# Performance work log

Hardware: AMD Instinct MI355X
Metric: run time of the kernel (lower is better)

The kernel has to match this reference:

```python
import jax, jax.numpy as jnp
import numpy as np

# Model dims (rexgen/WLN canonical hyperparameters)
B, N, MAXNB, NBONDS = 16, 100, 10, 120
AF, BF, H, BIN = 82, 6, 300, 11
DEPTH, K = 3, 80


def setup_inputs() -> dict:
    key = jax.random.key(0)
    ks = jax.random.split(key, 24)
    f32 = jnp.float32
    inp = {}
    inp["fatoms"] = jax.random.normal(ks[0], (B, N, AF), f32)
    inp["fbonds"] = jax.random.normal(ks[1], (B, NBONDS, BF), f32)
    inp["atom_nb"] = jax.random.randint(ks[2], (B, N, MAXNB), 0, N)
    inp["bond_nb"] = jax.random.randint(ks[3], (B, N, MAXNB), 0, NBONDS)
    inp["num_nbs"] = jnp.full((B, N), MAXNB, jnp.int32)
    inp["n_atoms"] = jnp.full((B,), N, jnp.int32)
    inp["binary_feats"] = jax.random.normal(ks[4], (B, N, N, BIN), f32)
    inp["mask_neis"] = (jax.random.uniform(ks[5], (B, N, MAXNB, 1)) > 0.2).astype(f32)
    inp["mask_atoms"] = jnp.ones((B, N, 1), f32)
    # sparse_idx enumerates all (sample, atom_i, atom_j) pairs in row-major order
    sb = jnp.repeat(jnp.arange(B), N * N)
    si = jnp.tile(jnp.repeat(jnp.arange(N), N), B)
    sj = jnp.tile(jnp.arange(N), B * N)
    inp["sparse_idx"] = jnp.stack([sb, si, sj], axis=1).astype(jnp.int32)

    def w(k, shape):
        return jax.random.normal(k, shape, f32) * 0.1

    # WLNet params
    inp["W_atom"] = w(ks[6], (AF, H))
    inp["W_nei_atom"] = w(ks[7], (H, H))
    inp["W_nei_bond"] = w(ks[8], (BF, H))
    inp["W_self"] = w(ks[9], (H, H))
    inp["W_U2"] = w(ks[10], (H + BF, H)); inp["b_U2"] = jnp.zeros((H,), f32)
    inp["W_U1"] = w(ks[11], (2 * H, H)); inp["b_U1"] = jnp.zeros((H,), f32)
    # Attention params
    inp["W_att_local"] = w(ks[12], (H, H))
    inp["W_att_bin"] = w(ks[13], (BIN, H)); inp["b_att"] = jnp.zeros((H,), f32)
    inp["W_att_score"] = w(ks[14], (H, 1)); inp["b_att_score"] = jnp.zeros((1,), f32)
    # ReactivityScoring params
    inp["W_pl"] = w(ks[15], (H, H))
    inp["W_pg"] = w(ks[16], (H, H))
    inp["W_pb"] = w(ks[17], (BIN, H)); inp["b_p"] = jnp.zeros((H,), f32)
    inp["W_out"] = w(ks[18], (H, 1)); inp["b_out"] = jnp.zeros((1,), f32)
    return inp


def _pair_scores(fatoms, fbonds, binary_feats, mask_neis, mask_atoms,
                 W_atom, W_nei_atom, W_nei_bond, W_self, W_U2, b_U2, W_U1, b_U1,
                 W_att_local, W_att_bin, b_att, W_att_score, b_att_score,
                 W_pl, W_pg, W_pb, b_p, W_out, b_out,
                 atom_nb, bond_nb, sparse_idx):
    bidx = jnp.arange(B)[:, None, None]
    # --- WLNet graph convolution ---
    h = jax.nn.relu(fatoms @ W_atom)                       # [B,N,H]
    local = h
    for _ in range(DEPTH):
        fnei_atom = h[bidx, atom_nb]                       # [B,N,MAXNB,H]
        fnei_bond = fbonds[bidx, bond_nb]                  # [B,N,MAXNB,BF]
        h_nei = (fnei_atom @ W_nei_atom) * (fnei_bond @ W_nei_bond)
        f_nei = (h_nei * mask_neis).sum(axis=2)            # [B,N,H]
        f_self = h @ W_self
        local = f_nei * f_self * mask_atoms                # kernel output
        nei_label = jax.nn.relu(jnp.concatenate([fnei_atom, fnei_bond], -1) @ W_U2 + b_U2)
        nei_label = (nei_label * mask_neis).sum(axis=2)
        h = jax.nn.relu(jnp.concatenate([h, nei_label], -1) @ W_U1 + b_U1)
    # --- Global attention over atom pairs ---
    pair = local[:, :, None, :] + local[:, None, :, :]     # [B,N,N,H]
    att_h = jax.nn.relu(pair @ W_att_local + binary_feats @ W_att_bin + b_att)
    att_s = jax.nn.sigmoid(att_h @ W_att_score + b_att_score)  # [B,N,N,1]
    ctx = jnp.einsum('bij,bjh->bih', att_s[..., 0], local)     # [B,N,H]
    # --- Gather sparse pairs and score reactivity ---
    sb, si, sj = sparse_idx[:, 0], sparse_idx[:, 1], sparse_idx[:, 2]
    local_pair = local[sb, si] + local[sb, sj]             # [P,H]
    global_pair = ctx[sb, si] + ctx[sb, sj]                # [P,H]
    bin_pair = binary_feats[sb, si, sj]                    # [P,BIN]
    hid = jax.nn.relu(local_pair @ W_pl + global_pair @ W_pg + bin_pair @ W_pb + b_p)
    return hid @ W_out + b_out                             # [P,1]


def reference(fatoms, fbonds, atom_nb, bond_nb, num_nbs, n_atoms, binary_feats,
              mask_neis, mask_atoms, sparse_idx,
              W_atom, W_nei_atom, W_nei_bond, W_self, W_U2, b_U2, W_U1, b_U1,
              W_att_local, W_att_bin, b_att, W_att_score, b_att_score,
              W_pl, W_pg, W_pb, b_p, W_out, b_out):
    pair_scores = _pair_scores(fatoms, fbonds, binary_feats, mask_neis, mask_atoms,
                               W_atom, W_nei_atom, W_nei_bond, W_self, W_U2, b_U2, W_U1, b_U1,
                               W_att_local, W_att_bin, b_att, W_att_score, b_att_score,
                               W_pl, W_pg, W_pb, b_p, W_out, b_out,
                               atom_nb, bond_nb, sparse_idx)
    # Segmented top-k: sparse_idx rows are grouped & ordered by sample with
    # exactly N*N pairs each, so per-sample flatten == reshape to [B, N*N].
    _, topks = jax.lax.top_k(pair_scores.reshape(B, N * N), K)  # indices, matching torch.topk[1]
    return pair_scores, topks
```

## Files before the change

### kernel.cpp

```cpp
#include <hip/hip_runtime.h>
#include <hip/hip_bf16.h>
#include <math.h>

#define BB 16
#define NN 100
#define MAXNB 10
#define NBONDS 120
#define AF 82
#define BF 6
#define HH 300
#define BIN 11
#define DEPTH 3
#define KTOP 80

typedef __attribute__((ext_vector_type(8))) short short8;
typedef __attribute__((ext_vector_type(4))) float floatx4;

__device__ __forceinline__ unsigned short f2bf(float f) {
    unsigned int u = __float_as_uint(f);
    unsigned int r = (u + 0x7FFFu + ((u >> 16) & 1u)) >> 16;
    return (unsigned short)r;
}
__device__ __forceinline__ float bf2f(unsigned short h) {
    return __uint_as_float(((unsigned int)h) << 16);
}

#define O_WATOM 0
#define O_WNB   29184
#define O_U2B   38912
#define O_WNA   48640
#define O_P1    145920
#define O_P2    243200
#define O_U1CAT 340480
#define O_WATT  535040
#define O_WPL   632320
#define O_WPG   729600

__global__ __launch_bounds__(256) void k_prep(
    const float* __restrict__ s0, const float* __restrict__ s1,
    const float* __restrict__ s2, const float* __restrict__ s3,
    const float* __restrict__ s4, const float* __restrict__ s5,
    const float* __restrict__ s6, const float* __restrict__ s7,
    const float* __restrict__ s8, const float* __restrict__ s9,
    const float* __restrict__ s10,
    unsigned short* __restrict__ WTh, unsigned short* __restrict__ WTl,
    const float* __restrict__ fatoms, const float* __restrict__ fbonds,
    unsigned short* __restrict__ fatomsbf, unsigned short* __restrict__ fbondsbf,
    const float* __restrict__ bin, unsigned short* __restrict__ BINBF,
    const float* __restrict__ Wbin0, const float* __restrict__ Wbin1,
    unsigned short* __restrict__ WBF0, unsigned short* __restrict__ WBF1)
{
    const int z = blockIdx.z;
    if (z == 11) {
        int idx = blockIdx.x * 256 + threadIdx.x;
        if (idx < 1600 * 96) {
            int r = idx / 96, c = idx - r * 96;
            float f = (c < AF) ? fatoms[r * AF + c] : 0.f;
            unsigned short hb = f2bf(f);
            fatomsbf[r * 192 + c]      = hb;
            fatomsbf[r * 192 + 96 + c] = f2bf(f - bf2f(hb));
        } else {
            int i2 = idx - 1600 * 96;
            if (i2 < 1920 * 32) {
                int r = i2 / 32, c = i2 - r * 32;
                float f = (c < BF) ? fbonds[r * BF + c] : 0.f;
                unsigned short hb = f2bf(f);
                fbondsbf[r * 64 + c]      = hb;
                fbondsbf[r * 64 + 32 + c] = f2bf(f - bf2f(hb));
            }
        }
        return;
    }
    if (z == 12) {
        const int bx = blockIdx.x;
        if (bx < 625) {
            int p = bx * 256 + threadIdx.x;
            if (p < BB * NN * NN) {
                const float* src = bin + (size_t)p * BIN;
                unsigned short tmp[16];
#pragma unroll
                for (int k = 0; k < BIN; k++) tmp[k] = f2bf(src[k]);
#pragma unroll
                for (int k = BIN; k < 16; k++) tmp[k] = 0;
                *(uint4*)(BINBF + (size_t)p * 16) = *(uint4*)tmp;
                *(uint4*)(BINBF + (size_t)p * 16 + 8) = *(uint4*)(tmp + 8);
            }
        } else if (bx < 663) {
            int zb = bx - 625;
            const float* src = (zb >= 19) ? Wbin1 : Wbin0;
            unsigned short* dst = (zb >= 19) ? WBF1 : WBF0;
            int idx = (zb % 19) * 256 + threadIdx.x;
            int jj = idx & 7;
            int koct = (idx >> 3) & 1;
            int n = (idx >> 4) & 15;
            int ch = idx >> 8;
            int k = koct * 8 + jj;
            int h = ch * 16 + n;
            float f = (k < BIN && h < 300) ? src[k * 300 + h] : 0.f;
            dst[idx] = f2bf(f);
        }
        return;
    }
    const float* src; int K, kc, off, u1base = -1;
    switch (z) {
        case 0:  src = s0;  K = AF;  kc = 3;  off = O_WATOM; break;
        case 1:  src = s1;  K = BF;  kc = 1;  off = O_WNB;   break;
        case 2:  src = s2;  K = BF;  kc = 1;  off = O_U2B;   break;
        case 3:  src = s3;  K = HH;  kc = 10; off = O_WNA;   break;
        case 4:  src = s4;  K = HH;  kc = 10; off = O_P1;    break;
        case 5:  src = s5;  K = HH;  kc = 10; off = O_P2;    break;
        case 6:  src = s6;  K = HH;  kc = 10; off = O_U1CAT; u1base = 0;  break;
        case 7:  src = s7;  K = HH;  kc = 10; off = O_U1CAT; u1base = 10; break;
        case 8:  src = s8;  K = HH;  kc = 10; off = O_WATT;  break;
        case 9:  src = s9;  K = HH;  kc = 10; off = O_WPL;   break;
        default: src = s10; K = HH;  kc = 10; off = O_WPG;   break;
    }
    const int lim = 9728 * kc;
    int i = blockIdx.x * 256 + threadIdx.x;
    if (i < lim) {
        int jj = i & 7;
        int lane = (i >> 3) & 63;
        int rem = i >> 9;
        int kci = rem % kc;
        int ct = rem / kc;
        int k = kci * 32 + (lane >> 4) * 8 + jj;
        int col = ct * 16 + (lane & 15);
        float f = (k < K && col < 300) ? src[k * 300 + col] : 0.f;
        unsigned short hb = f2bf(f);
        int dsti = (u1base >= 0)
                 ? off + ct * 10240 + (kci + u1base) * 512 + lane * 8 + jj
                 : off + i;
        WTh[dsti] = hb;
        WTl[dsti] = f2bf(f - bf2f(hb));
    }
}

__device__ __forceinline__ void gemm_epilogue(
    floatx4 acc, int ct, int m, int rq, int row0,
    float* __restrict__ C, int ldc, const float* __restrict__ bias,
    int act, unsigned short* __restrict__ Cbf, int gcolBase)
{
    const int col = ct * 16 + m;
    if (col >= 300) return;
    const float bv = bias ? bias[col] : 0.f;
    const int gcol = gcolBase + col;
#pragma unroll
    for (int r = 0; r < 4; r++) {
        const int grow = row0 + rq * 4 + r;
        float v = acc[r] + bv;
        if (act) v = fmaxf(v, 0.f);
        if (C) C[(size_t)grow * ldc + gcol] = v;
        if (Cbf) {
            unsigned short hb = f2bf(v);
            Cbf[(size_t)grow * 640 + col]       = hb;
            Cbf[(size_t)grow * 640 + 320 + col] = f2bf(v - bf2f(hb));
        }
    }
}

template<int KC>
__device__ __forceinline__ void gemm_core32(
    const unsigned short* __restrict__ A, int lda, int M,
    const unsigned short* __restrict__ wthB, const unsigned short* __restrict__ wtlB,
    float* __restrict__ C, int ldc,
    const float* __restrict__ bias,
    int act, unsigned short* __restrict__ Cbf,
    int row0, int gcolBase)
{
    constexpr int sR = KC * 64 + 8;
    __shared__ unsigned short sa[32 * sR];
    if (row0 >= M) return;
    const int tid = threadIdx.x;
    const int lane = tid & 63;
    const int wid = tid >> 6;

    {
        const uint4* Ag = (const uint4*)A;
        uint4* sa4 = (uint4*)sa;
        constexpr int q4 = KC * 8;
        const int lda4 = lda >> 3;
        constexpr int sR4 = q4 + 1;
        for (int i = tid; i < 32 * q4; i += 256) {
            int r = i / q4, q = i - r * q4;
            sa4[r * sR4 + q] = Ag[(size_t)(row0 + r) * lda4 + q];
        }
    }
    __syncthreads();

    const int ct = blockIdx.y * 4 + wid;
    if (ct >= 19) return;

    const int m = lane & 15;
    const int rq = lane >> 4;
    const int koct8 = rq * 8;
    const unsigned short* wth = wthB + (size_t)ct * KC * 512;
    const unsigned short* wtl = wtlB + (size_t)ct * KC * 512;

    floatx4 acc0 = {0.f, 0.f, 0.f, 0.f};
    floatx4 acc1 = {0.f, 0.f, 0.f, 0.f};
    for (int kci = 0; kci < KC; kci++) {
        short8 ah0 = *(const short8*)(sa + m * sR + kci * 32 + koct8);
        short8 al0 = *(const short8*)(sa + m * sR + KC * 32 + kci * 32 + koct8);
        short8 ah1 = *(const short8*)(sa + (16 + m) * sR + kci * 32 + koct8);
        short8 al1 = *(const short8*)(sa + (16 + m) * sR + KC * 32 + kci * 32 + koct8);
        short8 wh = *(const short8*)(wth + (kci * 64 + lane) * 8);
        short8 wl = *(const short8*)(wtl + (kci * 64 + lane) * 8);
        acc0 = __builtin_amdgcn_mfma_f32_16x16x32_bf16(ah0, wl, acc0, 0, 0, 0);
        acc1 = __builtin_amdgcn_mfma_f32_16x16x32_bf16(ah1, wl, acc1, 0, 0, 0);
        acc0 = __builtin_amdgcn_mfma_f32_16x16x32_bf16(al0, wh, acc0, 0, 0, 0);
        acc1 = __builtin_amdgcn_mfma_f32_16x16x32_bf16(al1, wh, acc1, 0, 0, 0);
        acc0 = __builtin_amdgcn_mfma_f32_16x16x32_bf16(ah0, wh, acc0, 0, 0, 0);
        acc1 = __builtin_amdgcn_mfma_f32_16x16x32_bf16(ah1, wh, acc1, 0, 0, 0);
    }

    gemm_epilogue(acc0, ct, m, rq, row0,      C, ldc, bias, act, Cbf, gcolBase);
    gemm_epilogue(acc1, ct, m, rq, row0 + 16, C, ldc, bias, act, Cbf, gcolBase);
}

__global__ __launch_bounds__(256) void k_gemm_mfma(
    const unsigned short* __restrict__ A, int lda, int M,
    const unsigned short* __restrict__ WTh, const unsigned short* __restrict__ WTl,
    int wtStride,
    float* __restrict__ C, int ldc,
    const float* __restrict__ bias,
    int act, unsigned short* __restrict__ Cbf)
{
    const int widx = blockIdx.z;
    gemm_core32<10>(A, lda, M,
              WTh + (size_t)widx * wtStride, WTl + (size_t)widx * wtStride,
              C, ldc, bias, act, Cbf,
              blockIdx.x * 32, widx * 300);
}

__global__ __launch_bounds__(256) void k_gemm_u1(
    const unsigned short* __restrict__ Ah,
    const unsigned short* __restrict__ An,
    const unsigned short* __restrict__ WTh, const unsigned short* __restrict__ WTl,
    const float* __restrict__ bias,
    unsigned short* __restrict__ Cbf)
{
    __shared__ unsigned short sa[16 * 1288];
    const int row0 = blockIdx.x * 16;
    if (row0 >= 1600) return;
    const int tid = threadIdx.x;
    const int lane = tid & 63;
    const int wid = tid >> 6;

    {
        const uint4* Ag = (const uint4*)Ah;
        const uint4* Ng = (const uint4*)An;
        uint4* sa4 = (uint4*)sa;
        for (int i = tid; i < 16 * 160; i += 256) {
            int r = i / 160, q = i - r * 160;
            const size_t rb = (size_t)(row0 + r) * 80;
            uint4 v;
            if (q < 40)       v = Ag[rb + q];
            else if (q < 80)  v = Ng[rb + (q - 40)];
            else if (q < 120) v = Ag[rb + (q - 40)];
            else              v = Ng[rb + (q - 80)];
            sa4[r * 161 + q] = v;
        }
    }
    __syncthreads();

    const int ct = blockIdx.y * 4 + wid;
    if (ct >= 19) return;

    const int m = lane & 15;
    const int rq = lane >> 4;
    const int koct8 = rq * 8;
    const unsigned short* wth = WTh + (size_t)ct * 10240;
    const unsigned short* wtl = WTl + (size_t)ct * 10240;

    floatx4 acc = {0.f, 0.f, 0.f, 0.f};
    for (int kci = 0; kci < 20; kci++) {
        short8 ah = *(const short8*)(sa + m * 1288 + kci * 32 + koct8);
        short8 al = *(const short8*)(sa + m * 1288 + 640 + kci * 32 + koct8);
        short8 wh = *(const short8*)(wth + (kci * 64 + lane) * 8);
        short8 wl = *(const short8*)(wtl + (kci * 64 + lane) * 8);
        acc = __builtin_amdgcn_mfma_f32_16x16x32_bf16(ah, wl, acc, 0, 0, 0);
        acc = __builtin_amdgcn_mfma_f32_16x16x32_bf16(al, wh, acc, 0, 0, 0);
        acc = __builtin_amdgcn_mfma_f32_16x16x32_bf16(ah, wh, acc, 0, 0, 0);
    }

    const int col = ct * 16 + m;
    if (col < 300) {
        const float bv = bias[col];
#pragma unroll
        for (int r = 0; r < 4; r++) {
            const int grow = row0 + rq * 4 + r;
            float v = fmaxf(acc[r] + bv, 0.f);
            unsigned short hb = f2bf(v);
            Cbf[(size_t)grow * 640 + col]       = hb;
            Cbf[(size_t)grow * 640 + 320 + col] = f2bf(v - bf2f(hb));
        }
    }
}

__global__ __launch_bounds__(256) void k_gemm_first(
    const unsigned short* __restrict__ fatomsbf,
    const unsigned short* __restrict__ fbondsbf,
    const unsigned short* __restrict__ WTh, const unsigned short* __restrict__ WTl,
    unsigned short* __restrict__ hbf, float* __restrict__ FBout)
{
    const int z = blockIdx.z;
    if (z == 0) {
        gemm_core32<3>(fatomsbf, 192, 1600,
                  WTh + O_WATOM, WTl + O_WATOM,
                  nullptr, 0, nullptr, 1, hbf,
                  blockIdx.x * 32, 0);
    } else {
        const int w = z - 1;
        gemm_core32<1>(fbondsbf, 64, 1920,
                  WTh + O_WNB + w * 9728, WTl + O_WNB + w * 9728,
                  FBout, 600, nullptr, 0, nullptr,
                  blockIdx.x * 32, w * 300);
    }
}

__global__ __launch_bounds__(320, 4) void k_neighbor(
    const float* __restrict__ HW, const float* __restrict__ FB,
    const int* __restrict__ atom_nb, const int* __restrict__ bond_nb,
    const float* __restrict__ mask_neis, const float* __restrict__ mask_atoms,
    const float* __restrict__ b_U2,
    unsigned short* __restrict__ localbf, unsigned short* __restrict__ nlbf,
    int computeU1)
{
    __shared__ int   sAn[2][MAXNB];
    __shared__ int   sBd[2][MAXNB];
    __shared__ float sM[2][MAXNB];
    __shared__ float pF[2][300];
    __shared__ float pN[2][300];
    const int tx = threadIdx.x;
    const int ty = threadIdx.y;
    const int tz = threadIdx.z;
    const int bx = blockIdx.x;
    const int bn0 = ((bx & 15) * 50 + (bx >> 4)) * 2;
    const int flat = (tz * 2 + ty) * 80 + tx;

    if (flat < 20)       sAn[flat / 10][flat % 10] = atom_nb[(bn0 + flat / 10) * MAXNB + flat % 10];
    else if (flat < 40)  { int f = flat - 20; sBd[f / 10][f % 10] = bond_nb[(bn0 + f / 10) * MAXNB + f % 10]; }
    else if (flat < 60)  { int f = flat - 40; sM[f / 10][f % 10]  = mask_neis[(bn0 + f / 10) * MAXNB + f % 10]; }
    __syncthreads();

    const int bn = bn0 + ty;
    const int b = bn / NN;
    const int h4 = tx;
    const float4* HW4 = (const float4*)HW;
    const float4* FB4 = (const float4*)FB;

    float4 fnei = make_float4(0.f, 0.f, 0.f, 0.f);
    float4 nls  = fnei;
    if (tx < 75) {
        if (computeU1) {
            const float4 bu = ((const float4*)b_U2)[h4];
#pragma unroll
            for (int kk = 0; kk < 5; kk++) {
                const int k = tz * 5 + kk;
                const int an = sAn[ty][k];
                const int bd = sBd[ty][k];
                const float m = sM[ty][k];
                const float4* hr = HW4 + (size_t)(b * NN + an) * 225;
                const float4* fr = FB4 + (size_t)(b * NBONDS + bd) * 150;
                float4 ha = hr[h4];
                float4 hu = hr[150 + h4];
                float4 fa = fr[h4];
                float4 fu = fr[75 + h4];
                fnei.x = fmaf(m, ha.x * fa.x, fnei.x);
                fnei.y = fmaf(m, ha.y * fa.y, fnei.y);
                fnei.z = fmaf(m, ha.z * fa.z, fnei.z);
                fnei.w = fmaf(m, ha.w * fa.w, fnei.w);
                float ux = hu.x + fu.x + bu.x;
                float uy = hu.y + fu.y + bu.y;
                float uz = hu.z + fu.z + bu.z;
                float uw = hu.w + fu.w + bu.w;
                nls.x = fmaf(m, fmaxf(ux, 0.f), nls.x);
                nls.y = fmaf(m, fmaxf(uy, 0.f), nls.y);
                nls.z = fmaf(m, fmaxf(uz, 0.f), nls.z);
                nls.w = fmaf(m, fmaxf(uw, 0.f), nls.w);
            }
        } else {
#pragma unroll
            for (int kk = 0; kk < 5; kk++) {
                const int k = tz * 5 + kk;
                const int an = sAn[ty][k];
                const int bd = sBd[ty][k];
                const float m = sM[ty][k];
                float4 ha = HW4[(size_t)(b * NN + an) * 225 + h4];
                float4 fa = FB4[(size_t)(b * NBONDS + bd) * 150 + h4];
                fnei.x = fmaf(m, ha.x * fa.x, fnei.x);
                fnei.y = fmaf(m, ha.y * fa.y, fnei.y);
                fnei.z = fmaf(m, ha.z * fa.z, fnei.z);
                fnei.w = fmaf(m, ha.w * fa.w, fnei.w);
            }
        }
        if (tz == 1) {
            ((float4*)pF[ty])[h4] = fnei;
            if (computeU1) ((float4*)pN[ty])[h4] = nls;
        }
    }
    __syncthreads();

    if (tx < 75 && tz == 0) {
        const float4 pf = ((const float4*)pF[ty])[h4];
        fnei.x += pf.x; fnei.y += pf.y; fnei.z += pf.z; fnei.w += pf.w;

        const float ma = mask_atoms[bn];
        const float4 sf = HW4[(size_t)bn * 225 + 75 + h4];
        float lv[4];
        lv[0] = fnei.x * sf.x * ma; lv[1] = fnei.y * sf.y * ma;
        lv[2] = fnei.z * sf.z * ma; lv[3] = fnei.w * sf.w * ma;

        ushort4 lh, ll;
        unsigned short* lhp = (unsigned short*)&lh;
        unsigned short* llp = (unsigned short*)&ll;
#pragma unroll
        for (int c = 0; c < 4; c++) {
            unsigned short hb = f2bf(lv[c]);
            lhp[c] = hb; llp[c] = f2bf(lv[c] - bf2f(hb));
        }
        *(ushort4*)(localbf + (size_t)bn * 640 + h4 * 4)       = lh;
        *(ushort4*)(localbf + (size_t)bn * 640 + 320 + h4 * 4) = ll;

        if (computeU1) {
            const float4 pn = ((const float4*)pN[ty])[h4];
            float nv[4] = {nls.x + pn.x, nls.y + pn.y, nls.z + pn.z, nls.w + pn.w};
            ushort4 nh, nl2;
            unsigned short* nhp = (unsigned short*)&nh;
            unsigned short* nlp = (unsigned short*)&nl2;
#pragma unroll
            for (int c = 0; c < 4; c++) {
                unsigned short nb = f2bf(nv[c]);
                nhp[c] = nb; nlp[c] = f2bf(nv[c] - bf2f(nb));
            }
            *(ushort4*)(nlbf + (size_t)bn * 640 + h4 * 4)       = nh;
            *(ushort4*)(nlbf + (size_t)bn * 640 + 320 + h4 * 4) = nl2;
        }
    }
}

__global__ __launch_bounds__(256) void k_pair(
    const float* __restrict__ R, int ldr,
    const unsigned short* __restrict__ BINBF,
    const unsigned short* __restrict__ WBF,
    const float* __restrict__ bvec,
    const float* __restrict__ Wscore, const float* __restrict__ bscore,
    float* __restrict__ outp, int mode)
{
    __shared__ float sLi[16 * 308];
    __shared__ float sLj[16 * 308];

    const int b  = blockIdx.x;
    const int i0 = blockIdx.y * 16;
    const int j0 = blockIdx.z * 16;
    const int tid = threadIdx.x;
    const int lane = tid & 63;
    const int wid = tid >> 6;

    for (int idx = tid; idx < 16 * 308; idx += 256) {
        int r = idx / 308;
        int c = idx - r * 308;
        float vi = 0.f, vj = 0.f;
        if (c < 300) {
            if (i0 + r < NN) vi = R[(size_t)(b * NN + i0 + r) * ldr + c] + bvec[c];
            if (j0 + r < NN) vj = R[(size_t)(b * NN + j0 + r) * ldr + c];
        }
        sLi[idx] = vi;
        sLj[idx] = vj;
    }

    const int m = lane & 15;
    const int koct = lane >> 4;
    short8 afrag[4];
#pragma unroll
    for (int g = 0; g < 4; g++) {
        int ii = i0 + wid * 4 + g; if (ii > NN - 1) ii = NN - 1;
        int jj2 = j0 + m;          if (jj2 > NN - 1) jj2 = NN - 1;
        const size_t pidx = (size_t)((b * NN + ii) * NN + jj2);
        afrag[g] = *(const short8*)(BINBF + pidx * 16 + (koct & 1) * 8);
        if (koct >= 2) afrag[g] = short8{0,0,0,0,0,0,0,0};
    }
    __syncthreads();

    const int n = lane & 15;
    const int rquad = lane >> 4;
    const floatx4 zero = {0.f, 0.f, 0.f, 0.f};
    float su[4][4];
#pragma unroll
    for (int g = 0; g < 4; g++)
#pragma unroll
        for (int r = 0; r < 4; r++) su[g][r] = 0.f;

    for (int ch = 0; ch < 19; ch++) {
        const int h0 = ch * 16;
        short8 bfrag = {0,0,0,0,0,0,0,0};
        if (lane < 32)
            bfrag = *(const short8*)(WBF + ch * 256 + (n * 2 + koct) * 8);
        float wsv = 0.f;
        if (h0 + n < 300) wsv = Wscore[h0 + n];
#pragma unroll
        for (int g = 0; g < 4; g++) {
            floatx4 P = __builtin_amdgcn_mfma_f32_16x16x32_bf16(
                afrag[g], bfrag, zero, 0, 0, 0);
            const float liv = sLi[(wid * 4 + g) * 308 + h0 + n];
#pragma unroll
            for (int r = 0; r < 4; r++) {
                const float ljv = sLj[(rquad * 4 + r) * 308 + h0 + n];
                float u = P[r] + liv + ljv;
                su[g][r] = fmaf(fmaxf(u, 0.f), wsv, su[g][r]);
            }
        }
    }

    const float bs = bscore[0];
#pragma unroll
    for (int g = 0; g < 4; g++) {
#pragma unroll
        for (int r = 0; r < 4; r++) {
            float v = su[g][r];
            v += __shfl_xor(v, 1);
            v += __shfl_xor(v, 2);
            v += __shfl_xor(v, 4);
            v += __shfl_xor(v, 8);
            if (n == 0) {
                const int i = i0 + wid * 4 + g;
                const int j = j0 + rquad * 4 + r;
                if (i < NN && j < NN) {
                    float s = v + bs;
                    outp[(size_t)(b * NN + i) * NN + j] =
                        (mode == 0) ? (1.f / (1.f + expf(-s))) : s;
                }
            }
        }
    }
}

__global__ __launch_bounds__(320, 2) void k_ctx(
    const float* __restrict__ att, const float* __restrict__ LL,
    float* __restrict__ LPG)
{
    const int bx = blockIdx.x;
    const int b = bx & 15;
    const int i0 = (bx >> 4) * 4;
    const int tid = threadIdx.x;
    __shared__ float sa[4 * NN];
    for (int idx = tid; idx < 4 * NN; idx += 320) {
        int ii = idx / NN, j = idx - ii * NN;
        sa[idx] = att[(size_t)(b * NN + i0 + ii) * NN + j];
    }
    __syncthreads();
    if (tid < HH) {
        float acc0 = 0.f, acc1 = 0.f, acc2 = 0.f, acc3 = 0.f;
#pragma unroll 4
        for (int j = 0; j < NN; j++) {
            const float lv = LL[(size_t)(b * NN + j) * 900 + 600 + tid];
            acc0 = fmaf(sa[j], lv, acc0);
            acc1 = fmaf(sa[NN + j], lv, acc1);
            acc2 = fmaf(sa[2 * NN + j], lv, acc2);
            acc3 = fmaf(sa[3 * NN + j], lv, acc3);
        }
        float vals[4] = {acc0, acc1, acc2, acc3};
#pragma unroll
        for (int k = 0; k < 4; k++) {
            LPG[(size_t)(b * NN + i0 + k) * 300 + tid] =
                vals[k] + LL[(size_t)(b * NN + i0 + k) * 900 + 300 + tid];
        }
    }
}

__global__ __launch_bounds__(1024) void k_topk(
    const float* __restrict__ scores, float* __restrict__ topk_out)
{
    const int b = blockIdx.x;
    const int tid = threadIdx.x;
    const int wid = tid >> 6;
    const int lane = tid & 63;
    const float* sc = scores + (size_t)b * (NN * NN);

    __shared__ unsigned int skey[NN * NN];
    __shared__ unsigned int whist[16 * 256];
    __shared__ unsigned int hist[256];
    __shared__ unsigned int candU[KTOP];
    __shared__ int candI[KTOP];
    __shared__ int cntG;
    __shared__ int curMin;
    __shared__ unsigned int sh_pref, sh_mask;
    __shared__ int sh_kRem;
    __shared__ int sh_last;

    for (int idx = tid; idx < NN * NN; idx += 1024) {
        unsigned int u = __float_as_uint(sc[idx]);
        u = (u & 0x80000000u) ? ~u : (u | 0x80000000u);
        skey[idx] = u;
    }
    if (tid == 0) {
        sh_pref = 0u; sh_mask = 0u; sh_kRem = KTOP; cntG = 0; sh_last = -1;
    }
    __syncthreads();

    for (int pass = 0; pass < 4; pass++) {
        const int shift = 24 - 8 * pass;
        unsigned int* wh = whist + (wid << 8);
        wh[lane] = 0u; wh[lane + 64] = 0u; wh[lane + 128] = 0u; wh[lane + 192] = 0u;
        __syncthreads();
        const unsigned int pref = sh_pref, mask = sh_mask;
        for (int idx = tid; idx < NN * NN; idx += 1024) {
            unsigned int u = skey[idx];
            if ((u & mask) == pref)
                atomicAdd(&wh[(u >> shift) & 255u], 1u);
        }
        __syncthreads();
        if (tid < 256) {
            unsigned int s = 0u;
#pragma unroll
            for (int w = 0; w < 16; w++) s += whist[(w << 8) | tid];
            hist[tid] = s;
        }
        __syncthreads();
        if (wid == 0) {
            unsigned int h0 = hist[lane * 4 + 0];
            unsigned int h1 = hist[lane * 4 + 1];
            unsigned int h2 = hist[lane * 4 + 2];
            unsigned int h3 = hist[lane * 4 + 3];
            unsigned int own = h0 + h1 + h2 + h3;
            unsigned int suf = own;
#pragma unroll
            for (int off = 1; off < 64; off <<= 1) {
                unsigned int v = __shfl_down(suf, off);
                if (lane + off < 64) suf += v;
            }
            const int k = sh_kRem;
            const unsigned int above = suf - own;
            if (above < (unsigned int)k && suf >= (unsigned int)k) {
                unsigned int c = above, hb; int bsel;
                c += h3;
                if ((int)c >= k) { bsel = lane * 4 + 3; hb = h3; }
                else { c += h2;
                    if ((int)c >= k) { bsel = lane * 4 + 2; hb = h2; }
                    else { c += h1;
                        if ((int)c >= k) { bsel = lane * 4 + 1; hb = h1; }
                        else { c += h0; bsel = lane * 4; hb = h0; } } }
                sh_kRem = k - (int)(c - hb);
                sh_pref = pref | ((unsigned int)bsel << shift);
                sh_mask = mask | (0xFFu << shift);
            }
        }
        __syncthreads();
    }
    const unsigned int T = sh_pref;

    for (int idx = tid; idx < NN * NN; idx += 1024) {
        unsigned int u = skey[idx];
        if (u > T) {
            int pos = atomicAdd(&cntG, 1);
            candU[pos] = u;
            candI[pos] = idx;
        }
    }
    __syncthreads();
    const int needE = KTOP - cntG;

    for (int e = 0; e < needE; e++) {
        if (tid == 0) curMin = 0x7fffffff;
        __syncthreads();
        const int last = sh_last;
        for (int idx = tid; idx < NN * NN; idx += 1024) {
            if (skey[idx] == T && idx > last)
                atomicMin(&curMin, idx);
        }
        __syncthreads();
        if (tid == 0) {
            candU[cntG + e] = T;
            candI[cntG + e] = curMin;
            sh_last = curMin;
        }
        __syncthreads();
    }

    if (tid < KTOP) {
        const unsigned int mu = candU[tid];
        const int mi = candI[tid];
        int rank = 0;
        for (int o = 0; o < KTOP; o++) {
            unsigned int ou = candU[o];
            int oi = candI[o];
            if (ou > mu || (ou == mu && oi < mi)) rank++;
        }
        topk_out[b * KTOP + rank] = (float)mi;
    }
}

extern "C" void kernel_launch(void* const* d_in, const int* in_sizes, int n_in,
                              void* d_out, int out_size, void* d_ws, size_t ws_size,
                              hipStream_t stream) {
    const float* fatoms       = (const float*)d_in[0];
    const float* fbonds       = (const float*)d_in[1];
    const int*   atom_nb      = (const int*)d_in[2];
    const int*   bond_nb      = (const int*)d_in[3];
    const float* binary_feats = (const float*)d_in[6];
    const float* mask_neis    = (const float*)d_in[7];
    const float* mask_atoms   = (const float*)d_in[8];
    const float* W_atom       = (const float*)d_in[10];
    const float* W_nei_atom   = (const float*)d_in[11];
    const float* W_nei_bond   = (const float*)d_in[12];
    const float* W_self       = (const float*)d_in[13];
    const float* W_U2         = (const float*)d_in[14];
    const float* b_U2         = (const float*)d_in[15];
    const float* W_U1         = (const float*)d_in[16];
    const float* b_U1         = (const float*)d_in[17];
    const float* W_att_local  = (const float*)d_in[18];
    const float* W_att_bin    = (const float*)d_in[19];
    const float* b_att        = (const float*)d_in[20];
    const float* W_att_score  = (const float*)d_in[21];
    const float* b_att_score  = (const float*)d_in[22];
    const float* W_pl         = (const float*)d_in[23];
    const float* W_pg         = (const float*)d_in[24];
    const float* W_pb         = (const float*)d_in[25];
    const float* b_p          = (const float*)d_in[26];
    const float* W_out        = (const float*)d_in[27];
    const float* b_out        = (const float*)d_in[28];

    float* ws = (float*)d_ws;
    float* HW  = ws;
    float* FB  = HW + 1440000;
    float* LL  = FB + 1152000;
    float* LPG = LL + 1440000;
    float* att = LPG + 480000;
    unsigned short* S0       = (unsigned short*)(ws + 4672000);
    unsigned short* hbf      = S0;
    unsigned short* hbf2     = S0 + 1024000;
    unsigned short* nlbf     = S0 + 2048000;
    unsigned short* localbf  = S0 + 3072000;
    unsigned short* WTh      = S0 + 4096000;
    unsigned short* WTl      = S0 + 4922880;
    unsigned short* BINBF    = S0 + 5749760;
    unsigned short* WBF_att  = S0 + 8309760;
    unsigned short* WBF_fin  = S0 + 8314624;
    unsigned short* fatomsbf = S0 + 8319488;
    unsigned short* fbondsbf = S0 + 8626688;

    float* out = (float*)d_out;
    float* topk_out = out + (size_t)BB * NN * NN;

    k_prep<<<dim3(840, 1, 13), 256, 0, stream>>>(
        W_atom, W_nei_bond, W_U2 + 300 * 300, W_nei_atom, W_self, W_U2,
        W_U1, W_U1 + 300 * 300, W_att_local, W_pl, W_pg, WTh, WTl,
        fatoms, fbonds, fatomsbf, fbondsbf,
        binary_feats, BINBF, W_att_bin, W_pb, WBF_att, WBF_fin);

    k_gemm_first<<<dim3(60, 5, 3), 256, 0, stream>>>(
        fatomsbf, fbondsbf, WTh, WTl, hbf, FB);

    unsigned short* hb[2] = {hbf, hbf2};
    int cur = 0;
    for (int d = 0; d < DEPTH; d++) {
        int nW = (d == DEPTH - 1) ? 2 : 3;
        k_gemm_mfma<<<dim3(50, 5, nW), 256, 0, stream>>>(
            hb[cur], 640, 1600, WTh + O_WNA, WTl + O_WNA, 97280,
            HW, 900, nullptr, 0, nullptr);
        k_neighbor<<<dim3(800), dim3(80, 2, 2), 0, stream>>>(
            HW, FB, atom_nb, bond_nb, mask_neis, mask_atoms, b_U2,
            localbf, nlbf, (d < DEPTH - 1) ? 1 : 0);
        if (d < DEPTH - 1) {
            k_gemm_u1<<<dim3(100, 5, 1), 256, 0, stream>>>(
                hb[cur], nlbf, WTh + O_U1CAT, WTl + O_U1CAT, b_U1, hb[cur ^ 1]);
            cur ^= 1;
        }
    }

    k_gemm_mfma<<<dim3(50, 5, 3), 256, 0, stream>>>(
        localbf, 640, 1600, WTh + O_WATT, WTl + O_WATT, 97280,
        LL, 900, nullptr, 0, nullptr);

    k_pair<<<dim3(16, 7, 7), 256, 0, stream>>>(
        LL, 900, BINBF, WBF_att, b_att, W_att_score, b_att_score,
        att, 0);

    k_ctx<<<dim3(BB * 25), 320, 0, stream>>>(att, LL, LPG);

    k_pair<<<dim3(16, 7, 7), 256, 0, stream>>>(
        LPG, 300, BINBF, WBF_fin, b_p, W_out, b_out,
        out, 1);

    k_topk<<<dim3(BB), 1024, 0, stream>>>(out, topk_out);
}
```

Measured before the change: 286.2 us.

## Compact prep grid to exact blocks and exit top-k radix passes early

The prep kernel now launches a flat 1D grid sized to the blocks each sub-task actually needs, in place of a 840x13 grid where most blocks exited at once. This removes launch and scheduling of idle blocks. The top-k kernel stops its radix histogram passes once the count of elements above the current bucket fits a 512-entry candidate buffer. It then ranks all collected candidates by brute force, which trades histogram passes and barriers for a larger O(n^2) rank step over up to 512 candidates.

New measurement: 286.5 us. No clear change (+0.1%).

```diff
diff --git a/kernel.cpp b/kernel.cpp
--- a/kernel.cpp
+++ b/kernel.cpp
@@ -50,9 +50,17 @@
     const float* __restrict__ Wbin0, const float* __restrict__ Wbin1,
     unsigned short* __restrict__ WBF0, unsigned short* __restrict__ WBF1)
 {
-    const int z = blockIdx.z;
+    const int bx0 = blockIdx.x;
+    int z, bxl;
+    if (bx0 < 114)       { z = 0;  bxl = bx0; }
+    else if (bx0 < 152)  { z = 1;  bxl = bx0 - 114; }
+    else if (bx0 < 190)  { z = 2;  bxl = bx0 - 152; }
+    else if (bx0 < 3230) { int t = bx0 - 190; z = 3 + t / 380; bxl = t % 380; }
+    else if (bx0 < 4070) { z = 11; bxl = bx0 - 3230; }
+    else                 { z = 12; bxl = bx0 - 4070; }
+
     if (z == 11) {
-        int idx = blockIdx.x * 256 + threadIdx.x;
+        int idx = bxl * 256 + threadIdx.x;
         if (idx < 1600 * 96) {
             int r = idx / 96, c = idx - r * 96;
             float f = (c < AF) ? fatoms[r * AF + c] : 0.f;
@@ -72,9 +80,8 @@
         return;
     }
     if (z == 12) {
-        const int bx = blockIdx.x;
-        if (bx < 625) {
-            int p = bx * 256 + threadIdx.x;
+        if (bxl < 625) {
+            int p = bxl * 256 + threadIdx.x;
             if (p < BB * NN * NN) {
                 const float* src = bin + (size_t)p * BIN;
                 unsigned short tmp[16];
@@ -85,8 +92,8 @@
                 *(uint4*)(BINBF + (size_t)p * 16) = *(uint4*)tmp;
                 *(uint4*)(BINBF + (size_t)p * 16 + 8) = *(uint4*)(tmp + 8);
             }
-        } else if (bx < 663) {
-            int zb = bx - 625;
+        } else if (bxl < 663) {
+            int zb = bxl - 625;
             const float* src = (zb >= 19) ? Wbin1 : Wbin0;
             unsigned short* dst = (zb >= 19) ? WBF1 : WBF0;
             int idx = (zb % 19) * 256 + threadIdx.x;
@@ -116,7 +123,7 @@
         default: src = s10; K = HH;  kc = 10; off = O_WPG;   break;
     }
     const int lim = 9728 * kc;
-    int i = blockIdx.x * 256 + threadIdx.x;
+    int i = bxl * 256 + threadIdx.x;
     if (i < lim) {
         int jj = i & 7;
         int lane = (i >> 3) & 63;
@@ -568,6 +575,7 @@
     }
 }
 
+#define TCAP 512
 __global__ __launch_bounds__(1024) void k_topk(
     const float* __restrict__ scores, float* __restrict__ topk_out)
 {
@@ -580,13 +588,14 @@
     __shared__ unsigned int skey[NN * NN];
     __shared__ unsigned int whist[16 * 256];
     __shared__ unsigned int hist[256];
-    __shared__ unsigned int candU[KTOP];
-    __shared__ int candI[KTOP];
+    __shared__ unsigned int candU[TCAP];
+    __shared__ int candI[TCAP];
     __shared__ int cntG;
     __shared__ int curMin;
     __shared__ unsigned int sh_pref, sh_mask;
     __shared__ int sh_kRem;
     __shared__ int sh_last;
+    __shared__ int sh_hb;
 
     for (int idx = tid; idx < NN * NN; idx += 1024) {
         unsigned int u = __float_as_uint(sc[idx]);
@@ -595,6 +604,7 @@
     }
     if (tid == 0) {
         sh_pref = 0u; sh_mask = 0u; sh_kRem = KTOP; cntG = 0; sh_last = -1;
+        sh_hb = 0x7fffffff;
     }
     __syncthreads();
 
@@ -643,9 +653,11 @@
                 sh_kRem = k - (int)(c - hb);
                 sh_pref = pref | ((unsigned int)bsel << shift);
                 sh_mask = mask | (0xFFu << shift);
+                sh_hb = (int)hb;
             }
         }
         __syncthreads();
+        if (sh_hb <= TCAP - KTOP) break;
     }
     const unsigned int T = sh_pref;
 
@@ -653,12 +665,12 @@
         unsigned int u = skey[idx];
         if (u > T) {
             int pos = atomicAdd(&cntG, 1);
-            candU[pos] = u;
-            candI[pos] = idx;
+            if (pos < TCAP) { candU[pos] = u; candI[pos] = idx; }
         }
     }
     __syncthreads();
-    const int needE = KTOP - cntG;
+    const int cg = (cntG < TCAP) ? cntG : TCAP;
+    const int needE = KTOP - cg;
 
     for (int e = 0; e < needE; e++) {
         if (tid == 0) curMin = 0x7fffffff;
@@ -670,23 +682,25 @@
         }
         __syncthreads();
         if (tid == 0) {
-            candU[cntG + e] = T;
-            candI[cntG + e] = curMin;
+            candU[cg + e] = T;
+            candI[cg + e] = curMin;
             sh_last = curMin;
         }
         __syncthreads();
     }
 
-    if (tid < KTOP) {
+    const int nc = (cg < KTOP) ? KTOP : cg;
+    if (tid < nc) {
         const unsigned int mu = candU[tid];
         const int mi = candI[tid];
         int rank = 0;
-        for (int o = 0; o < KTOP; o++) {
+        for (int o = 0; o < nc; o++) {
             unsigned int ou = candU[o];
             int oi = candI[o];
             if (ou > mu || (ou == mu && oi < mi)) rank++;
         }
-        topk_out[b * KTOP + rank] = (float)mi;
+        if (rank < KTOP)
+            topk_out[b * KTOP + rank] = (float)mi;
     }
 }
 
@@ -742,7 +756,7 @@
     float* out = (float*)d_out;
     float* topk_out = out + (size_t)BB * NN * NN;
 
-    k_prep<<<dim3(840, 1, 13), 256, 0, stream>>>(
+    k_prep<<<dim3(4733), 256, 0, stream>>>(
         W_atom, W_nei_bond, W_U2 + 300 * 300, W_nei_atom, W_self, W_U2,
         W_U1, W_U1 + 300 * 300, W_att_local, W_pl, W_pg, WTh, WTl,
         fatoms, fbonds, fatomsbf, fbondsbf,
```
